# Optimization experiments

Measured on AMD Instinct MI355X. Metric: run time of the kernel, lower is better.

Reference implementation:

```python
import jax, jax.numpy as jnp
import numpy as np

TILE = 64        # tile_hw -> P = TILE*TILE = 4096 rays per image
N_GAUSS = 16384
N_CAMS = 8
N_IMGS = 2
EPS = 1e-5


def setup_inputs() -> dict:
    key = jax.random.key(0)
    k1, k2, k3, k4, k5, k6 = jax.random.split(key, 6)
    means = jax.random.normal(k1, (N_GAUSS, 3), dtype=jnp.float32)
    # covariances only used through their diagonal mean; keep diagonals positive
    covs = jax.random.uniform(k2, (N_GAUSS, 3, 3), dtype=jnp.float32, minval=0.05, maxval=1.0)
    colors = jax.random.uniform(k3, (N_GAUSS, 3), dtype=jnp.float32)
    fx = fy = 70.0
    cx = cy = TILE / 2.0
    intrinsics = jnp.tile(jnp.array([fx, fy, cx, cy], dtype=jnp.float32), (N_CAMS, 1))
    # extrinsics: identity rotation, camera ~4 units along +z with jitter, looking toward -z
    trans = jnp.concatenate(
        [0.5 * jax.random.normal(k4, (N_CAMS, 2)),
         4.0 + 0.2 * jax.random.normal(k5, (N_CAMS, 1))], axis=-1).astype(jnp.float32)
    extrinsics = jnp.broadcast_to(jnp.eye(4, dtype=jnp.float32), (N_CAMS, 4, 4))
    extrinsics = extrinsics.at[:, :3, 3].set(trans)
    image_ids = jax.random.randint(k6, (N_IMGS,), 0, N_CAMS)
    return {"means": means, "covs": covs, "colors": colors,
            "intrinsics": intrinsics, "extrinsics": extrinsics, "image_ids": image_ids}


def _render_one(means, covs, colors, intr, c2w):
    fx, fy, cx, cy = intr[0], intr[1], intr[2], intr[3]
    # ray generation (matches torch meshgrid indexing='xy')
    i, j = jnp.meshgrid(jnp.arange(TILE, dtype=jnp.float32),
                        jnp.arange(TILE, dtype=jnp.float32), indexing='xy')
    dirs = jnp.stack([(i - cx) / fx, -(j - cy) / fy, -jnp.ones_like(i)], axis=-1)  # [H,W,3]
    Rrot = c2w[:3, :3]
    rays_d = jnp.einsum('hwk,jk->hwj', dirs, Rrot).reshape(-1, 3)   # [P,3] = dirs @ R^T
    rays_o = jnp.broadcast_to(c2w[:3, 3], rays_d.shape)             # [P,3]

    # per-ray gaussian distance weights (attention-like score)
    diff = means[None, :, :] - rays_o[:, None, :]                   # [P,N,3]
    t = jnp.sum(diff * rays_d[:, None, :], axis=-1, keepdims=True)  # [P,N,1]
    closest = rays_o[:, None, :] + rays_d[:, None, :] * t           # [P,N,3]
    pdiff = means[None, :, :] - closest                             # [P,N,3]
    sigma = jnp.sqrt(jnp.mean(jnp.diagonal(covs, axis1=1, axis2=2), axis=1))  # [N]
    dist2 = jnp.sum(pdiff ** 2, axis=-1)                            # [P,N]
    weights = jnp.exp(-0.5 * dist2 / (sigma[None, :] ** 2 + EPS))   # [P,N]

    # weighted color aggregation + normalization (softmax-like value aggregation)
    rgb = (weights @ colors) / (jnp.sum(weights, axis=-1, keepdims=True) + EPS)  # [P,3]
    return rgb.T.reshape(3, TILE * TILE)


def reference(means, covs, colors, intrinsics, extrinsics, image_ids):
    cam_i = intrinsics[image_ids]   # [B,4]
    cam_e = extrinsics[image_ids]   # [B,4,4]
    render = lambda intr, c2w: _render_one(means, covs, colors, intr, c2w)
    return jax.vmap(render)(cam_i, cam_e)   # [B, 3, TILE*TILE]
```

## Files before the change

### kernel.cpp

```cpp
#include <hip/hip_runtime.h>

#define N_GAUSS 16384
#define SPLIT   128
#define GPS     (N_GAUSS / SPLIT)
#define TILE    64
#define NPIX    (TILE * TILE)
#define PPT     2
#define EPS     1e-5f
#define LOG2E   1.44269504088896340736f

__global__ __launch_bounds__(256, 8) void render_kernel(
        const float* __restrict__ means,
        const float* __restrict__ covs,
        const float* __restrict__ colors,
        const float* __restrict__ intr,
        const float* __restrict__ extr,
        const int*   __restrict__ img_ids,
        float4*      __restrict__ partial) {
    __shared__ float4 sA[GPS];
    __shared__ float4 sB[GPS];

    const int tid   = threadIdx.x;
    const int split = blockIdx.y;
    const int img   = blockIdx.z;
    const int n_imgs = gridDim.z;

    const int cam = img_ids[img];
    const float* E = extr + 16 * cam;
    const float ox = E[3], oy = E[7], oz = E[11];

    if (tid < GPS) {
        const int g = split * GPS + tid;
        const float mx = means[3 * g + 0];
        const float my = means[3 * g + 1];
        const float mz = means[3 * g + 2];
        const float* c = covs + 9 * g;
        const float s2  = (c[0] + c[4] + c[8]) * (1.0f / 3.0f);
        const float sig = sqrtf(s2);
        const float kg2 = -0.5f * LOG2E / (sig * sig + EPS);
        const float sg  = sqrtf(-kg2);
        const float ux = mx - ox, uy = my - oy, uz = mz - oz;
        const float e0 = kg2 * (ux * ux + uy * uy + uz * uz);
        sA[tid] = make_float4(mx, my, mz, sg);
        sB[tid] = make_float4(colors[3 * g + 0], colors[3 * g + 1],
                              colors[3 * g + 2], e0);
    }

    const float* I = intr + 4 * cam;
    const float fx = I[0], fy = I[1], cx = I[2], cy = I[3];

    float rdx[PPT], rdy[PPT], rdz[PPT], mods[PPT];
    int pix[PPT];
    #pragma unroll
    for (int p = 0; p < PPT; p++) {
        pix[p] = blockIdx.x * 256 + tid + p * (NPIX / PPT);
        const int row = pix[p] >> 6;
        const int col = pix[p] & 63;
        const float d0 = ((float)col - cx) / fx;
        const float d1 = -(((float)row) - cy) / fy;
        const float d2 = -1.0f;
        const float x = d0 * E[0] + d1 * E[1] + d2 * E[2];
        const float y = d0 * E[4] + d1 * E[5] + d2 * E[6];
        const float z = d0 * E[8] + d1 * E[9] + d2 * E[10];
        const float dd2 = x * x + y * y + z * z - 2.0f;
        const float sp  = sqrtf(-dd2);
        rdx[p] = x * sp; rdy[p] = y * sp; rdz[p] = z * sp;
        mods[p] = -(ox * x + oy * y + oz * z) * sp;
    }

    __syncthreads();

    float w0 = 0.f, r0 = 0.f, g0 = 0.f, b0 = 0.f;
    float w1 = 0.f, r1 = 0.f, g1 = 0.f, b1 = 0.f;
    #pragma unroll 4
    for (int g = 0; g < GPS; g++) {
        const float4 a = sA[g];
        const float4 b = sB[g];
        const float t0 = fmaf(a.x, rdx[0], fmaf(a.y, rdy[0], fmaf(a.z, rdz[0], mods[0])));
        const float t1 = fmaf(a.x, rdx[1], fmaf(a.y, rdy[1], fmaf(a.z, rdz[1], mods[1])));
        const float u0 = t0 * a.w;
        const float u1 = t1 * a.w;
        const float e_0 = __builtin_amdgcn_exp2f(fmaf(u0, u0, b.w));
        const float e_1 = __builtin_amdgcn_exp2f(fmaf(u1, u1, b.w));
        w0 += e_0; r0 = fmaf(e_0, b.x, r0); g0 = fmaf(e_0, b.y, g0); b0 = fmaf(e_0, b.z, b0);
        w1 += e_1; r1 = fmaf(e_1, b.x, r1); g1 = fmaf(e_1, b.y, g1); b1 = fmaf(e_1, b.z, b1);
    }

    const int stride = n_imgs * NPIX;
    float4* P = partial + (size_t)split * stride + img * NPIX;
    P[pix[0]] = make_float4(w0, r0, g0, b0);
    P[pix[1]] = make_float4(w1, r1, g1, b1);
}

__global__ void reduce_kernel(const float4* __restrict__ partial,
                              float* __restrict__ out,
                              int n_imgs) {
    const int idx = blockIdx.x * blockDim.x + threadIdx.x;
    const int total = n_imgs * NPIX;
    if (idx >= total) return;
    float w = 0.0f, r = 0.0f, g = 0.0f, b = 0.0f;
    #pragma unroll 8
    for (int s = 0; s < SPLIT; s++) {
        const float4 p = partial[(size_t)s * total + idx];
        w += p.x; r += p.y; g += p.z; b += p.w;
    }
    const float inv = 1.0f / (w + EPS);
    const int img = idx >> 12;
    const int pix = idx & (NPIX - 1);
    out[(img * 3 + 0) * NPIX + pix] = r * inv;
    out[(img * 3 + 1) * NPIX + pix] = g * inv;
    out[(img * 3 + 2) * NPIX + pix] = b * inv;
}

extern "C" void kernel_launch(void* const* d_in, const int* in_sizes, int n_in,
                              void* d_out, int out_size, void* d_ws, size_t ws_size,
                              hipStream_t stream) {
    const float* means   = (const float*)d_in[0];
    const float* covs    = (const float*)d_in[1];
    const float* colors  = (const float*)d_in[2];
    const float* intr    = (const float*)d_in[3];
    const float* extr    = (const float*)d_in[4];
    const int*   img_ids = (const int*)d_in[5];
    float* out = (float*)d_out;
    const int n_imgs = in_sizes[5];

    float4* partial = (float4*)d_ws;

    dim3 grid(NPIX / (256 * PPT), SPLIT, n_imgs);
    render_kernel<<<grid, 256, 0, stream>>>(means, covs, colors, intr, extr,
                                            img_ids, partial);

    const int total = n_imgs * NPIX;
    reduce_kernel<<<(total + 255) / 256, 256, 0, stream>>>(partial, out, n_imgs);
}
```

Measured before the change: 106.3 us.

## Use packed FP32 math with four pixels per thread in render loop

Each thread now handles four pixels instead of two, stored as pairs of 2-wide float vectors so the compiler can emit packed FP32 FMA/mul instructions (v_pk_fma_f32) for the projection and accumulation. The exp2 calls stay scalar. Grid x shrinks by half and the occupancy hint drops from 8 to 4 blocks per CU to allow more registers. The goal is fewer VALU issue slots per Gaussian-pixel pair and fewer LDS reads per pixel, at the cost of lower occupancy and fewer blocks.

After: 104.2 us. -2.0%, faster.

```diff
diff --git a/kernel.cpp b/kernel.cpp
--- a/kernel.cpp
+++ b/kernel.cpp
@@ -5,11 +5,13 @@
 #define GPS     (N_GAUSS / SPLIT)
 #define TILE    64
 #define NPIX    (TILE * TILE)
-#define PPT     2
+#define PPT     4
 #define EPS     1e-5f
 #define LOG2E   1.44269504088896340736f
 
-__global__ __launch_bounds__(256, 8) void render_kernel(
+typedef float v2f __attribute__((ext_vector_type(2)));
+
+__global__ __launch_bounds__(256, 4) void render_kernel(
         const float* __restrict__ means,
         const float* __restrict__ covs,
         const float* __restrict__ colors,
@@ -49,7 +51,7 @@
     const float* I = intr + 4 * cam;
     const float fx = I[0], fy = I[1], cx = I[2], cy = I[3];
 
-    float rdx[PPT], rdy[PPT], rdz[PPT], mods[PPT];
+    v2f rx[2], ry[2], rz[2], md[2];
     int pix[PPT];
     #pragma unroll
     for (int p = 0; p < PPT; p++) {
@@ -64,32 +66,51 @@
         const float z = d0 * E[8] + d1 * E[9] + d2 * E[10];
         const float dd2 = x * x + y * y + z * z - 2.0f;
         const float sp  = sqrtf(-dd2);
-        rdx[p] = x * sp; rdy[p] = y * sp; rdz[p] = z * sp;
-        mods[p] = -(ox * x + oy * y + oz * z) * sp;
+        rx[p >> 1][p & 1] = x * sp;
+        ry[p >> 1][p & 1] = y * sp;
+        rz[p >> 1][p & 1] = z * sp;
+        md[p >> 1][p & 1] = -(ox * x + oy * y + oz * z) * sp;
     }
 
     __syncthreads();
 
-    float w0 = 0.f, r0 = 0.f, g0 = 0.f, b0 = 0.f;
-    float w1 = 0.f, r1 = 0.f, g1 = 0.f, b1 = 0.f;
+    v2f wv[2] = {{0.f, 0.f}, {0.f, 0.f}};
+    v2f rv[2] = {{0.f, 0.f}, {0.f, 0.f}};
+    v2f gv[2] = {{0.f, 0.f}, {0.f, 0.f}};
+    v2f bv[2] = {{0.f, 0.f}, {0.f, 0.f}};
+
     #pragma unroll 4
     for (int g = 0; g < GPS; g++) {
         const float4 a = sA[g];
         const float4 b = sB[g];
-        const float t0 = fmaf(a.x, rdx[0], fmaf(a.y, rdy[0], fmaf(a.z, rdz[0], mods[0])));
-        const float t1 = fmaf(a.x, rdx[1], fmaf(a.y, rdy[1], fmaf(a.z, rdz[1], mods[1])));
-        const float u0 = t0 * a.w;
-        const float u1 = t1 * a.w;
-        const float e_0 = __builtin_amdgcn_exp2f(fmaf(u0, u0, b.w));
-        const float e_1 = __builtin_amdgcn_exp2f(fmaf(u1, u1, b.w));
-        w0 += e_0; r0 = fmaf(e_0, b.x, r0); g0 = fmaf(e_0, b.y, g0); b0 = fmaf(e_0, b.z, b0);
-        w1 += e_1; r1 = fmaf(e_1, b.x, r1); g1 = fmaf(e_1, b.y, g1); b1 = fmaf(e_1, b.z, b1);
+        const v2f ax = {a.x, a.x}, ay = {a.y, a.y}, az = {a.z, a.z};
+        const v2f sgv = {a.w, a.w};
+        const v2f e0v = {b.w, b.w};
+        const v2f bxx = {b.x, b.x}, byy = {b.y, b.y}, bzz = {b.z, b.z};
+        #pragma unroll
+        for (int h = 0; h < 2; h++) {
+            const v2f t = __builtin_elementwise_fma(ax, rx[h],
+                          __builtin_elementwise_fma(ay, ry[h],
+                          __builtin_elementwise_fma(az, rz[h], md[h])));
+            const v2f u = t * sgv;
+            const v2f arg = __builtin_elementwise_fma(u, u, e0v);
+            v2f e;
+            e.x = __builtin_amdgcn_exp2f(arg.x);
+            e.y = __builtin_amdgcn_exp2f(arg.y);
+            wv[h] += e;
+            rv[h] = __builtin_elementwise_fma(e, bxx, rv[h]);
+            gv[h] = __builtin_elementwise_fma(e, byy, gv[h]);
+            bv[h] = __builtin_elementwise_fma(e, bzz, bv[h]);
+        }
     }
 
     const int stride = n_imgs * NPIX;
     float4* P = partial + (size_t)split * stride + img * NPIX;
-    P[pix[0]] = make_float4(w0, r0, g0, b0);
-    P[pix[1]] = make_float4(w1, r1, g1, b1);
+    #pragma unroll
+    for (int p = 0; p < PPT; p++) {
+        const int h = p >> 1, l = p & 1;
+        P[pix[p]] = make_float4(wv[h][l], rv[h][l], gv[h][l], bv[h][l]);
+    }
 }
 
 __global__ void reduce_kernel(const float4* __restrict__ partial,
```
